# Kernel tuning notes

Measured on AMD Instinct MI355X. Metric: run time of the kernel, lower is better.

## Reference

```python
import jax, jax.numpy as jnp
import numpy as np


def setup_inputs() -> dict:
    key = jax.random.key(0)
    ks = jax.random.split(key, 10)
    B, C1, C2, Co, H, W = 4, 128, 128, 128, 64, 64
    Cin = C1 + C2
    delta_p_processed = jax.random.normal(ks[0], (B, C1, H, W), jnp.float32)
    delta_f_hist = jax.random.normal(ks[1], (B, C2, H, W), jnp.float32)
    Wq = jax.random.normal(ks[2], (Co, Cin), jnp.float32) * 0.02
    bq = jax.random.normal(ks[3], (Co,), jnp.float32) * 0.02
    Wk = jax.random.normal(ks[4], (Co, Cin), jnp.float32) * 0.02
    bk = jax.random.normal(ks[5], (Co,), jnp.float32) * 0.02
    Wv = jax.random.normal(ks[6], (Co, Cin), jnp.float32) * 0.02
    bv = jax.random.normal(ks[7], (Co,), jnp.float32) * 0.02
    Wg = jax.random.normal(ks[8], (Co, Co), jnp.float32) * 0.02
    bg = jnp.zeros((Co,), jnp.float32)
    gamma = jnp.array([0.5], jnp.float32)
    return {
        "delta_p_processed": delta_p_processed,
        "delta_f_hist": delta_f_hist,
        "Wq": Wq, "bq": bq, "Wk": Wk, "bk": bk,
        "Wv": Wv, "bv": bv, "Wg": Wg, "bg": bg,
        "gamma": gamma,
    }


def reference(delta_p_processed, delta_f_hist, Wq, bq, Wk, bk, Wv, bv, Wg, bg, gamma):
    x = jnp.concatenate([delta_p_processed, delta_f_hist], axis=1)  # (B, Cin, H, W)
    B, Cin, H, W = x.shape
    Co = Wq.shape[0]
    N = H * W
    xf = x.reshape(B, Cin, N)
    # 1x1 convs == per-pixel linear projections
    q = jnp.einsum('oc,bcn->bno', Wq, xf) + bq          # (B, N, Co)
    k = jnp.einsum('oc,bcn->bon', Wk, xf) + bk[:, None]  # (B, Co, N)
    v = jnp.einsum('oc,bcn->bno', Wv, xf) + bv          # (B, N, Co)
    scale = 1.0 / (Co ** 0.5)
    attn = jax.nn.softmax(jnp.einsum('bno,bom->bnm', q, k) * scale, axis=-1)  # (B, N, N)
    out_attn = jnp.einsum('bnm,bmo->bno', attn, v)      # (B, N, Co)
    out_attn = out_attn.transpose(0, 2, 1).reshape(B, Co, H, W)
    gate = jax.nn.sigmoid(
        jnp.einsum('oc,bchw->bohw', Wg, out_attn) + bg[None, :, None, None]
    )
    residual = x[:, :Co, :, :]
    return gamma[0] * gate * out_attn + (1.0 - gate) * residual
```

## Files before the change

### kernel.cpp

```cpp
#include <hip/hip_runtime.h>
#include <stdint.h>

#define B_    4
#define CIN   256
#define CO    128
#define NPOS  4096

typedef float  f4      __attribute__((ext_vector_type(4)));
typedef float  f2      __attribute__((ext_vector_type(2)));
typedef float  f32x16  __attribute__((ext_vector_type(16)));
typedef int    int4v   __attribute__((ext_vector_type(4)));
typedef short  short4v __attribute__((ext_vector_type(4)));
typedef short  short8v __attribute__((ext_vector_type(8)));
typedef __bf16 bf16x8  __attribute__((ext_vector_type(8)));

#if __has_builtin(__builtin_amdgcn_exp2f)
#define EXP2(x) __builtin_amdgcn_exp2f(x)
#else
#define EXP2(x) exp2f(x)
#endif

static __device__ __forceinline__ unsigned short f2bf(float f){
  union { float f; unsigned int u; } v; v.f = f;
  unsigned int u = v.u + 0x7FFFu + ((v.u >> 16) & 1u);
  return (unsigned short)(u >> 16);
}
static __device__ __forceinline__ float bf2f(unsigned short h){
  union { unsigned int u; float f; } v; v.u = ((unsigned int)h) << 16;
  return v.f;
}
static __device__ __forceinline__ unsigned int cvt_pk_bf16(float lo, float hi){
  unsigned int r;
  asm("v_cvt_pk_bf16_f32 %0, %1, %2" : "=v"(r) : "v"(lo), "v"(hi));
  return r;
}

static __device__ __forceinline__ void half_swap_pair(float v, float& x, float& y){
  union { float f; int i; } a; a.f = v;
  auto r = __builtin_amdgcn_permlane32_swap(a.i, a.i, false, false);
  union { int i; float f; } o0, o1; o0.i = (int)r[0]; o1.i = (int)r[1];
  x = o0.f; y = o1.f;
}

__global__ __launch_bounds__(64) void wconv_kernel(
    const float* __restrict__ Wq, const float* __restrict__ Wk,
    const float* __restrict__ Wv, const float* __restrict__ Wg,
    unsigned short* __restrict__ Wf)
{
  int blk = blockIdx.x, l = threadIdx.x;
  const float* W; int o, c; int stride;
  if (blk < 192){
    int ob = blk >> 4, cs = blk & 15;
    int mat = ob >> 2, obl = ob & 3;
    W = (mat == 0) ? Wq : ((mat == 1) ? Wk : Wv);
    o = obl * 32 + (l & 31); c = cs * 16 + (l >> 5) * 8; stride = 256;
  } else {
    int idx = blk - 192;
    int ob = idx >> 3, cs = idx & 7;
    W = Wg;
    o = ob * 32 + (l & 31); c = cs * 16 + (l >> 5) * 8; stride = 128;
  }
  const float* src = W + (size_t)o * stride + c;
  f4 a = *(const f4*)src, bb = *(const f4*)(src + 4);
  short8v pk;
  #pragma unroll
  for (int j = 0; j < 4; ++j){ pk[j] = (short)f2bf(a[j]); pk[4+j] = (short)f2bf(bb[j]); }
  *(short8v*)(Wf + ((size_t)blk * 64 + l) * 8) = pk;
}

__global__ __launch_bounds__(256) void qkv_kernel(
    const float* __restrict__ dp, const float* __restrict__ df,
    const unsigned short* __restrict__ Wf,
    const float* __restrict__ bq, const float* __restrict__ bk,
    const float* __restrict__ bv,
    unsigned short* __restrict__ Qf, unsigned short* __restrict__ Kf,
    unsigned short* __restrict__ Vf)
{
  __shared__ unsigned int xs4[32 * 128];

  int t  = threadIdx.x;
  int b  = blockIdx.x >> 7;
  int kt = blockIdx.x & 127;
  int n0 = kt * 32;

  {
    int cp = t & 127, nh = t >> 7;
    int c0 = cp * 2, c1 = c0 + 1;
    const float* s0 = (c0 < 128) ? dp + ((size_t)b*128 + c0) * NPOS
                                 : df + ((size_t)b*128 + (c0-128)) * NPOS;
    const float* s1 = (c1 < 128) ? dp + ((size_t)b*128 + c1) * NPOS
                                 : df + ((size_t)b*128 + (c1-128)) * NPOS;
    f4 x0[4], x1[4];
    #pragma unroll
    for (int i = 0; i < 4; ++i){
      x0[i] = *(const f4*)(s0 + n0 + nh*16 + i*4);
      x1[i] = *(const f4*)(s1 + n0 + nh*16 + i*4);
    }
    #pragma unroll
    for (int i = 0; i < 16; ++i){
      int n = nh * 16 + i;
      unsigned int pk = cvt_pk_bf16(x0[i>>2][i&3], x1[i>>2][i&3]);
      int chunk = (cp >> 2) ^ (n & 7);
      xs4[n * 128 + chunk * 4 + (cp & 3)] = pk;
    }
  }
  __syncthreads();

  int w = t >> 6, l = t & 63;
  int lo5 = l & 31, h = l >> 5;

  f32x16 acc[3] = {};
  const unsigned short* WfL = Wf + (size_t)l * 8;

  #pragma unroll 4
  for (int cs = 0; cs < 16; ++cs){
    bf16x8 xf = *(const bf16x8*)((const char*)xs4 +
                 (size_t)(lo5 * 512 + (((cs*2 + h) ^ (lo5 & 7)) * 16)));
    #pragma unroll
    for (int i = 0; i < 3; ++i){
      int ob = w * 3 + i;
      bf16x8 wf = *(const bf16x8*)(WfL + ((size_t)ob * 16 + cs) * 512);
      if (ob < 8) acc[i] = __builtin_amdgcn_mfma_f32_32x32x16_bf16(wf, xf, acc[i], 0, 0, 0);
      else        acc[i] = __builtin_amdgcn_mfma_f32_32x32x16_bf16(xf, wf, acc[i], 0, 0, 0);
    }
  }

  const float kScale = 0.12751743f;
  #pragma unroll
  for (int i = 0; i < 3; ++i){
    int ob = w * 3 + i, mat = ob >> 2, obl = ob & 3;
    if (mat < 2){
      const float* bias = (mat == 0) ? bq : bk;
      unsigned short* dst = ((mat == 0) ? Qf : Kf) + (size_t)(b*128 + kt) * 4096;
      #pragma unroll
      for (int r1 = 0; r1 < 4; ++r1){
        f4 b4 = *(const f4*)(bias + obl*32 + r1*8 + h*4);
        float v0 = acc[i][r1*4+0] + b4[0], v1 = acc[i][r1*4+1] + b4[1];
        float v2 = acc[i][r1*4+2] + b4[2], v3 = acc[i][r1*4+3] + b4[3];
        if (mat == 0){ v0 *= kScale; v1 *= kScale; v2 *= kScale; v3 *= kScale; }
        union { unsigned int u[2]; short4v s; } pk;
        pk.u[0] = cvt_pk_bf16(v0, v1); pk.u[1] = cvt_pk_bf16(v2, v3);
        int ci = obl * 2 + (r1 >> 1);
        size_t si = (size_t)ci * 512 + (size_t)(lo5 + 32*(r1 & 1)) * 8 + 4*h;
        *(short4v*)(dst + si) = pk.s;
      }
    } else {
      float bvl = bv[obl * 32 + lo5];
      unsigned short* dst = Vf + ((size_t)(b*128 + kt) * 8 + obl*2) * 512;
      #pragma unroll
      for (int r1 = 0; r1 < 4; ++r1){
        union { unsigned int u[2]; short4v s; } pk;
        pk.u[0] = cvt_pk_bf16(acc[i][r1*4+0] + bvl, acc[i][r1*4+1] + bvl);
        pk.u[1] = cvt_pk_bf16(acc[i][r1*4+2] + bvl, acc[i][r1*4+3] + bvl);
        size_t si = (size_t)(r1 >> 1) * 512 + (size_t)(lo5 + 32*(r1 & 1)) * 8 + 4*h;
        *(short4v*)(dst + si) = pk.s;
      }
    }
  }
}

#define PIPE_TILE(T, CUR, NXT)                                                  \
  {                                                                             \
                 \
    {                                                                           \
      int t2_ = (T) + 2; if (t2_ >= NIT) t2_ -= NIT;                            \
      int t1_ = (T) + 1; if (t1_ >= NIT) t1_ -= NIT;                            \
      size_t tbK_ = (size_t)(kt0 + t2_) * 4096;                                 \
      size_t tbV_ = (size_t)(kt0 + t1_) * 4096;                                 \
      _Pragma("unroll")                                                         \
      for (int ci = 0; ci < 8; ++ci)                                            \
        kf[NXT][ci] = *(const bf16x8*)(KfL + tbK_ + ci * 512);                  \
      _Pragma("unroll")                                                         \
      for (int fi = 0; fi < 8; ++fi)                                            \
        vf[NXT][fi] = *(const bf16x8*)(VfL + tbV_ + fi * 512);                  \
    }                                                                           \
                    \
    f32x16 sA = {}, sB = {};                                                    \
    __builtin_amdgcn_s_setprio(1);                                              \
    _Pragma("unroll")                                                           \
    for (int ci = 0; ci < 4; ++ci){                                             \
      sA = __builtin_amdgcn_mfma_f32_32x32x16_bf16(kf[CUR][2*ci],   qf[2*ci],   sA, 0, 0, 0); \
      sB = __builtin_amdgcn_mfma_f32_32x32x16_bf16(kf[CUR][2*ci+1], qf[2*ci+1], sB, 0, 0, 0); \
    }                                                                           \
    __builtin_amdgcn_s_setprio(0);                                              \
         \
    float a0_ = fmaxf(fmaxf(sv[0],  sv[1]),  sv[2]);                            \
    float a1_ = fmaxf(fmaxf(sv[3],  sv[4]),  sv[5]);                            \
    float a2_ = fmaxf(fmaxf(sv[6],  sv[7]),  sv[8]);                            \
    float a3_ = fmaxf(fmaxf(sv[9],  sv[10]), sv[11]);                           \
    float a4_ = fmaxf(fmaxf(sv[12], sv[13]), sv[14]);                           \
    float vm  = fmaxf(fmaxf(fmaxf(fmaxf(a0_, a1_), a2_), fmaxf(a3_, a4_)), sv[15]); \
    { float xx_, yy_; half_swap_pair(vm, xx_, yy_);                             \
      vm = fmaxf(vm, fmaxf(xx_, yy_)); }                                        \
    if (!__all(vm <= m_run + 8.0f)){                                            \
      float m_new = fmaxf(m_run, vm);                                           \
      float alpha = EXP2(m_run - m_new);                                        \
      _Pragma("unroll")                                                         \
      for (int ob = 0; ob < 4; ++ob){                                           \
        _Pragma("unroll")                                                       \
        for (int i = 0; i < 16; ++i) oacc[ob][i] *= alpha;                      \
      }                                                                         \
      l_run *= alpha;                                                           \
      m_run = m_new;                                                            \
    }                                                                           \
    float p[16];                                                                \
    _Pragma("unroll")                                                           \
    for (int i = 0; i < 16; ++i) p[i] = EXP2(sv[i] - m_run);                    \
    float t0 = (p[0]  + p[1])  + (p[2]  + p[3]);                                \
    float t1 = (p[4]  + p[5])  + (p[6]  + p[7]);                                \
    float t2 = (p[8]  + p[9])  + (p[10] + p[11]);                               \
    float t3 = (p[12] + p[13]) + (p[14] + p[15]);                               \
    float ts = (t0 + t1) + (t2 + t3);                                           \
    { float xx_, yy_; half_swap_pair(ts, xx_, yy_); ts = xx_ + yy_; }           \
    l_run += ts;                                                                \
    unsigned int pw[8];                                                         \
    _Pragma("unroll")                                                           \
    for (int i = 0; i < 8; ++i) pw[i] = cvt_pk_bf16(p[2*i], p[2*i+1]);          \
    auto r20 = __builtin_amdgcn_permlane32_swap((int)pw[2], (int)pw[0], false, false); \
    auto r31 = __builtin_amdgcn_permlane32_swap((int)pw[3], (int)pw[1], false, false); \
    auto r64v = __builtin_amdgcn_permlane32_swap((int)pw[6], (int)pw[4], false, false); \
    auto r75 = __builtin_amdgcn_permlane32_swap((int)pw[7], (int)pw[5], false, false); \
    union { int4v i4; bf16x8 b; } pb0, pb1;                                     \
    pb0.i4 = (int4v){(int)r20[1],  (int)r31[1], (int)r20[0],  (int)r31[0]};     \
    pb1.i4 = (int4v){(int)r64v[1], (int)r75[1], (int)r64v[0], (int)r75[0]};     \
                                                     \
    __builtin_amdgcn_s_setprio(1);                                              \
    _Pragma("unroll")                                                           \
    for (int ob = 0; ob < 4; ++ob){                                             \
      oacc[ob] = __builtin_amdgcn_mfma_f32_32x32x16_bf16(vf[CUR][2*ob],   pb0.b, oacc[ob], 0, 0, 0); \
      oacc[ob] = __builtin_amdgcn_mfma_f32_32x32x16_bf16(vf[CUR][2*ob+1], pb1.b, oacc[ob], 0, 0, 0); \
    }                                                                           \
    __builtin_amdgcn_s_setprio(0);                                              \
              \
    sv = sA + sB;                                                               \
  }

__global__ __launch_bounds__(256) void attn_kernel(
    const unsigned short* __restrict__ Qf, const unsigned short* __restrict__ Kf,
    const unsigned short* __restrict__ Vf, float* __restrict__ OP,
    f2* __restrict__ ML, int SPLIT, int CHUNK)
{
  int t    = threadIdx.x;
  int s    = blockIdx.x % SPLIT;
  int rest = blockIdx.x / SPLIT;
  int b    = rest >> 5;
  int qb   = rest & 31;
  int w    = t >> 6;
  int l    = t & 63;
  int lq   = l & 31;
  int h    = l >> 5;
  int q0   = qb * 128 + w * 32;

  const unsigned short* QfL = Qf + (size_t)b * (128 * 8 * 512) + (size_t)l * 8;
  size_t qtb = (size_t)(q0 >> 5) * 4096;
  bf16x8 qf[8];
  #pragma unroll
  for (int ci = 0; ci < 8; ++ci) qf[ci] = *(const bf16x8*)(QfL + qtb + ci * 512);

  const unsigned short* KfL = Kf + (size_t)b * (128 * 8 * 512) + (size_t)l * 8;
  const unsigned short* VfL = Vf + (size_t)b * (128 * 8 * 512) + (size_t)l * 8;

  f32x16 oacc[4] = {};
  float m_run = -3.0e38f, l_run = 0.f;

  const int kt0 = (s * CHUNK) >> 5;
  const int NIT = CHUNK >> 5;

  bf16x8 kf[2][8];
  bf16x8 vf[2][8];
  {
    size_t tb0 = (size_t)kt0 * 4096;
    #pragma unroll
    for (int ci = 0; ci < 8; ++ci) kf[1][ci] = *(const bf16x8*)(KfL + tb0 + ci * 512);
    #pragma unroll
    for (int fi = 0; fi < 8; ++fi) vf[0][fi] = *(const bf16x8*)(VfL + tb0 + fi * 512);
    size_t tb1 = (size_t)(kt0 + 1) * 4096;
    #pragma unroll
    for (int ci = 0; ci < 8; ++ci) kf[0][ci] = *(const bf16x8*)(KfL + tb1 + ci * 512);
  }
  f32x16 sv;
  {
    f32x16 sA = {}, sB = {};
    #pragma unroll
    for (int ci = 0; ci < 4; ++ci){
      sA = __builtin_amdgcn_mfma_f32_32x32x16_bf16(kf[1][2*ci],   qf[2*ci],   sA, 0, 0, 0);
      sB = __builtin_amdgcn_mfma_f32_32x32x16_bf16(kf[1][2*ci+1], qf[2*ci+1], sB, 0, 0, 0);
    }
    sv = sA + sB;
  }

  for (int it = 0; it < NIT; it += 2){
    PIPE_TILE(it, 0, 1)
    PIPE_TILE(it + 1, 1, 0)
  }

  float* Ob = OP + (((size_t)b * NPOS + q0 + lq) * SPLIT + s) * 128 + h * 4;
  #pragma unroll
  for (int ob = 0; ob < 4; ++ob){
    #pragma unroll
    for (int rg = 0; rg < 4; ++rg){
      f4 vv;
      vv[0] = oacc[ob][rg*4+0]; vv[1] = oacc[ob][rg*4+1];
      vv[2] = oacc[ob][rg*4+2]; vv[3] = oacc[ob][rg*4+3];
      *(f4*)(Ob + ob * 32 + rg * 8) = vv;
    }
  }
  if (h == 0){
    f2 ml; ml[0] = m_run; ml[1] = l_run;
    ML[((size_t)b * NPOS + q0 + lq) * SPLIT + s] = ml;
  }
}

__global__ __launch_bounds__(256) void gate_kernel(
    const float* __restrict__ OP, const f2* __restrict__ ML,
    const unsigned short* __restrict__ Wf,
    const float* __restrict__ bg,
    const float* __restrict__ gamma, const float* __restrict__ dp,
    float* __restrict__ out, int SPLIT)
{
  __shared__ float        oat[128 * 33];
  __shared__ unsigned int xs[32 * 64];
  __shared__ float        wsm[32 * 8];

  int t  = threadIdx.x;
  int b  = blockIdx.x >> 7;
  int nt = blockIdx.x & 127;
  int n0 = nt * 32;

  if (t < 32){
    size_t mlb = ((size_t)b * NPOS + n0 + t) * SPLIT;
    float mmax = -3.0e38f;
    for (int sp = 0; sp < SPLIT; ++sp) mmax = fmaxf(mmax, ML[mlb + sp][0]);
    float L = 0.f;
    for (int sp = 0; sp < SPLIT; ++sp) L += ML[mlb + sp][1] * EXP2(ML[mlb + sp][0] - mmax);
    float Linv = 1.0f / L;
    for (int sp = 0; sp < SPLIT; ++sp)
      wsm[t * 8 + sp] = EXP2(ML[mlb + sp][0] - mmax) * Linv;
  }
  __syncthreads();

  int w = t >> 6, l = t & 63;

  #pragma unroll
  for (int i = 0; i < 8; ++i){
    int n = w * 8 + i;
    const f2* op = (const f2*)(OP + (((size_t)b * NPOS + n0 + n) * SPLIT) * 128) + l;
    float a0 = 0.f, a1 = 0.f;
    for (int sp = 0; sp < SPLIT; ++sp){
      f2 v = op[sp * 64];
      float ww = wsm[n * 8 + sp];
      a0 += ww * v[0]; a1 += ww * v[1];
    }
    oat[(2*l)   * 33 + n] = a0;
    oat[(2*l+1) * 33 + n] = a1;
    xs[n * 64 + (((l >> 2) ^ (n & 7)) << 2) + (l & 3)] = cvt_pk_bf16(a0, a1);
  }
  __syncthreads();

  int lq = l & 31, h = l >> 5;
  f32x16 acc = {};
  const unsigned short* WgfL = Wf + (size_t)(192 + w * 8) * 512 + (size_t)l * 8;
  #pragma unroll
  for (int cs = 0; cs < 8; ++cs){
    bf16x8 xf = *(const bf16x8*)((const char*)xs +
                 (size_t)(lq * 256 + (((cs*2 + h) ^ (lq & 7)) * 16)));
    bf16x8 wgf = *(const bf16x8*)(WgfL + (size_t)cs * 512);
    acc = __builtin_amdgcn_mfma_f32_32x32x16_bf16(wgf, xf, acc, 0, 0, 0);
  }

  float gm = gamma[0];
  const float kLog2e = 1.4426950408889634f;
  #pragma unroll
  for (int r1 = 0; r1 < 4; ++r1){
    f4 b4 = *(const f4*)(bg + w*32 + r1*8 + h*4);
    #pragma unroll
    for (int j = 0; j < 4; ++j){
      int o = w*32 + r1*8 + h*4 + j;
      float garg = acc[r1*4 + j] + b4[j];
      float gate = 1.0f / (1.0f + EXP2(-kLog2e * garg));
      float oa = oat[o * 33 + lq];
      size_t gi = ((size_t)b * 128 + o) * NPOS + n0 + lq;
      float rs = dp[gi];
      out[gi] = gm * gate * oa + (1.0f - gate) * rs;
    }
  }
}

extern "C" void kernel_launch(void* const* d_in, const int* in_sizes, int n_in,
                              void* d_out, int out_size, void* d_ws, size_t ws_size,
                              hipStream_t stream)
{
  (void)in_sizes; (void)n_in; (void)out_size;
  const float* dp    = (const float*)d_in[0];
  const float* df    = (const float*)d_in[1];
  const float* Wq    = (const float*)d_in[2];
  const float* bq    = (const float*)d_in[3];
  const float* Wk    = (const float*)d_in[4];
  const float* bk    = (const float*)d_in[5];
  const float* Wv    = (const float*)d_in[6];
  const float* bv    = (const float*)d_in[7];
  const float* Wg    = (const float*)d_in[8];
  const float* bg    = (const float*)d_in[9];
  const float* gamma = (const float*)d_in[10];

  const int SPLIT = 4;
  const int CHUNK = NPOS / SPLIT;

  unsigned short* Qf = (unsigned short*)d_ws;
  unsigned short* Kf = Qf + (size_t)B_ * NPOS * 128;
  unsigned short* Vf = Kf + (size_t)B_ * NPOS * 128;
  float*          OP = (float*)(Vf + (size_t)B_ * NPOS * 128);
  f2*             ML = (f2*)(OP + (size_t)B_ * NPOS * SPLIT * 128);
  unsigned short* Wf = (unsigned short*)(ML + (size_t)B_ * NPOS * SPLIT);
  float*          out = (float*)d_out;
  (void)ws_size;

  wconv_kernel<<<dim3(224), dim3(64), 0, stream>>>(Wq, Wk, Wv, Wg, Wf);
  qkv_kernel<<<dim3(B_ * 128), dim3(256), 0, stream>>>(dp, df, Wf, bq, bk, bv, Qf, Kf, Vf);
  attn_kernel<<<dim3(B_ * 32 * SPLIT), dim3(256), 0, stream>>>(Qf, Kf, Vf, OP, ML, SPLIT, CHUNK);
  gate_kernel<<<dim3(B_ * 128), dim3(256), 0, stream>>>(OP, ML, Wf, bg, gamma, dp, out, SPLIT);
}
```

Baseline: 94.56 us.

## Process two key tiles per iteration and compute softmax row sums via MFMA

Replaces the software-pipelined single-tile loop, which prefetched the next K and V tiles into register double buffers, with an unpipelined loop that handles two key tiles per iteration and shares one max/rescale check between them. The softmax denominator is now accumulated by extra MFMAs against a ones vector on the bf16 probabilities, replacing the scalar sums and cross-lane reductions. This cuts VALU reduction work and per-tile control overhead, but it loses the explicit load/compute overlap and adds MFMA work and register pressure. The row sum now uses bf16-rounded probabilities, which slightly changes numerics.

After: 99.93 us. 5.7% more time.

```diff
diff --git a/kernel.cpp b/kernel.cpp
--- a/kernel.cpp
+++ b/kernel.cpp
@@ -159,82 +159,6 @@
   }
 }
 
-#define PIPE_TILE(T, CUR, NXT)                                                  \
-  {                                                                             \
-                 \
-    {                                                                           \
-      int t2_ = (T) + 2; if (t2_ >= NIT) t2_ -= NIT;                            \
-      int t1_ = (T) + 1; if (t1_ >= NIT) t1_ -= NIT;                            \
-      size_t tbK_ = (size_t)(kt0 + t2_) * 4096;                                 \
-      size_t tbV_ = (size_t)(kt0 + t1_) * 4096;                                 \
-      _Pragma("unroll")                                                         \
-      for (int ci = 0; ci < 8; ++ci)                                            \
-        kf[NXT][ci] = *(const bf16x8*)(KfL + tbK_ + ci * 512);                  \
-      _Pragma("unroll")                                                         \
-      for (int fi = 0; fi < 8; ++fi)                                            \
-        vf[NXT][fi] = *(const bf16x8*)(VfL + tbV_ + fi * 512);                  \
-    }                                                                           \
-                    \
-    f32x16 sA = {}, sB = {};                                                    \
-    __builtin_amdgcn_s_setprio(1);                                              \
-    _Pragma("unroll")                                                           \
-    for (int ci = 0; ci < 4; ++ci){                                             \
-      sA = __builtin_amdgcn_mfma_f32_32x32x16_bf16(kf[CUR][2*ci],   qf[2*ci],   sA, 0, 0, 0); \
-      sB = __builtin_amdgcn_mfma_f32_32x32x16_bf16(kf[CUR][2*ci+1], qf[2*ci+1], sB, 0, 0, 0); \
-    }                                                                           \
-    __builtin_amdgcn_s_setprio(0);                                              \
-         \
-    float a0_ = fmaxf(fmaxf(sv[0],  sv[1]),  sv[2]);                            \
-    float a1_ = fmaxf(fmaxf(sv[3],  sv[4]),  sv[5]);                            \
-    float a2_ = fmaxf(fmaxf(sv[6],  sv[7]),  sv[8]);                            \
-    float a3_ = fmaxf(fmaxf(sv[9],  sv[10]), sv[11]);                           \
-    float a4_ = fmaxf(fmaxf(sv[12], sv[13]), sv[14]);                           \
-    float vm  = fmaxf(fmaxf(fmaxf(fmaxf(a0_, a1_), a2_), fmaxf(a3_, a4_)), sv[15]); \
-    { float xx_, yy_; half_swap_pair(vm, xx_, yy_);                             \
-      vm = fmaxf(vm, fmaxf(xx_, yy_)); }                                        \
-    if (!__all(vm <= m_run + 8.0f)){                                            \
-      float m_new = fmaxf(m_run, vm);                                           \
-      float alpha = EXP2(m_run - m_new);                                        \
-      _Pragma("unroll")                                                         \
-      for (int ob = 0; ob < 4; ++ob){                                           \
-        _Pragma("unroll")                                                       \
-        for (int i = 0; i < 16; ++i) oacc[ob][i] *= alpha;                      \
-      }                                                                         \
-      l_run *= alpha;                                                           \
-      m_run = m_new;                                                            \
-    }                                                                           \
-    float p[16];                                                                \
-    _Pragma("unroll")                                                           \
-    for (int i = 0; i < 16; ++i) p[i] = EXP2(sv[i] - m_run);                    \
-    float t0 = (p[0]  + p[1])  + (p[2]  + p[3]);                                \
-    float t1 = (p[4]  + p[5])  + (p[6]  + p[7]);                                \
-    float t2 = (p[8]  + p[9])  + (p[10] + p[11]);                               \
-    float t3 = (p[12] + p[13]) + (p[14] + p[15]);                               \
-    float ts = (t0 + t1) + (t2 + t3);                                           \
-    { float xx_, yy_; half_swap_pair(ts, xx_, yy_); ts = xx_ + yy_; }           \
-    l_run += ts;                                                                \
-    unsigned int pw[8];                                                         \
-    _Pragma("unroll")                                                           \
-    for (int i = 0; i < 8; ++i) pw[i] = cvt_pk_bf16(p[2*i], p[2*i+1]);          \
-    auto r20 = __builtin_amdgcn_permlane32_swap((int)pw[2], (int)pw[0], false, false); \
-    auto r31 = __builtin_amdgcn_permlane32_swap((int)pw[3], (int)pw[1], false, false); \
-    auto r64v = __builtin_amdgcn_permlane32_swap((int)pw[6], (int)pw[4], false, false); \
-    auto r75 = __builtin_amdgcn_permlane32_swap((int)pw[7], (int)pw[5], false, false); \
-    union { int4v i4; bf16x8 b; } pb0, pb1;                                     \
-    pb0.i4 = (int4v){(int)r20[1],  (int)r31[1], (int)r20[0],  (int)r31[0]};     \
-    pb1.i4 = (int4v){(int)r64v[1], (int)r75[1], (int)r64v[0], (int)r75[0]};     \
-                                                     \
-    __builtin_amdgcn_s_setprio(1);                                              \
-    _Pragma("unroll")                                                           \
-    for (int ob = 0; ob < 4; ++ob){                                             \
-      oacc[ob] = __builtin_amdgcn_mfma_f32_32x32x16_bf16(vf[CUR][2*ob],   pb0.b, oacc[ob], 0, 0, 0); \
-      oacc[ob] = __builtin_amdgcn_mfma_f32_32x32x16_bf16(vf[CUR][2*ob+1], pb1.b, oacc[ob], 0, 0, 0); \
-    }                                                                           \
-    __builtin_amdgcn_s_setprio(0);                                              \
-              \
-    sv = sA + sB;                                                               \
-  }
-
 __global__ __launch_bounds__(256) void attn_kernel(
     const unsigned short* __restrict__ Qf, const unsigned short* __restrict__ Kf,
     const unsigned short* __restrict__ Vf, float* __restrict__ OP,
@@ -261,37 +185,119 @@
   const unsigned short* VfL = Vf + (size_t)b * (128 * 8 * 512) + (size_t)l * 8;
 
   f32x16 oacc[4] = {};
-  float m_run = -3.0e38f, l_run = 0.f;
+  f32x16 lacc = {};
+  float m_run = -3.0e38f;
+
+  union { int4v i4; bf16x8 b; } ones_u;
+  ones_u.i4 = (int4v){0x3F803F80, 0x3F803F80, 0x3F803F80, 0x3F803F80};
+  bf16x8 ones = ones_u.b;
 
   const int kt0 = (s * CHUNK) >> 5;
   const int NIT = CHUNK >> 5;
 
-  bf16x8 kf[2][8];
-  bf16x8 vf[2][8];
-  {
-    size_t tb0 = (size_t)kt0 * 4096;
-    #pragma unroll
-    for (int ci = 0; ci < 8; ++ci) kf[1][ci] = *(const bf16x8*)(KfL + tb0 + ci * 512);
-    #pragma unroll
-    for (int fi = 0; fi < 8; ++fi) vf[0][fi] = *(const bf16x8*)(VfL + tb0 + fi * 512);
-    size_t tb1 = (size_t)(kt0 + 1) * 4096;
-    #pragma unroll
-    for (int ci = 0; ci < 8; ++ci) kf[0][ci] = *(const bf16x8*)(KfL + tb1 + ci * 512);
-  }
-  f32x16 sv;
-  {
-    f32x16 sA = {}, sB = {};
-    #pragma unroll
-    for (int ci = 0; ci < 4; ++ci){
-      sA = __builtin_amdgcn_mfma_f32_32x32x16_bf16(kf[1][2*ci],   qf[2*ci],   sA, 0, 0, 0);
-      sB = __builtin_amdgcn_mfma_f32_32x32x16_bf16(kf[1][2*ci+1], qf[2*ci+1], sB, 0, 0, 0);
-    }
-    sv = sA + sB;
-  }
-
   for (int it = 0; it < NIT; it += 2){
-    PIPE_TILE(it, 0, 1)
-    PIPE_TILE(it + 1, 1, 0)
+    size_t tbA = (size_t)(kt0 + it) * 4096;
+    size_t tbB = tbA + 4096;
+
+    bf16x8 kfA[8], kfB[8];
+    #pragma unroll
+    for (int ci = 0; ci < 8; ++ci){
+      kfA[ci] = *(const bf16x8*)(KfL + tbA + ci * 512);
+      kfB[ci] = *(const bf16x8*)(KfL + tbB + ci * 512);
+    }
+    f32x16 svA = {}, svB = {};
+    __builtin_amdgcn_s_setprio(1);
+    #pragma unroll
+    for (int ci = 0; ci < 8; ++ci){
+      svA = __builtin_amdgcn_mfma_f32_32x32x16_bf16(kfA[ci], qf[ci], svA, 0, 0, 0);
+      svB = __builtin_amdgcn_mfma_f32_32x32x16_bf16(kfB[ci], qf[ci], svB, 0, 0, 0);
+    }
+    __builtin_amdgcn_s_setprio(0);
+
+    bf16x8 vfA[8], vfB[8];
+    #pragma unroll
+    for (int fi = 0; fi < 8; ++fi){
+      vfA[fi] = *(const bf16x8*)(VfL + tbA + fi * 512);
+      vfB[fi] = *(const bf16x8*)(VfL + tbB + fi * 512);
+    }
+
+    float mA, mB;
+    { float a0_ = fmaxf(fmaxf(svA[0],  svA[1]),  svA[2]);
+      float a1_ = fmaxf(fmaxf(svA[3],  svA[4]),  svA[5]);
+      float a2_ = fmaxf(fmaxf(svA[6],  svA[7]),  svA[8]);
+      float a3_ = fmaxf(fmaxf(svA[9],  svA[10]), svA[11]);
+      float a4_ = fmaxf(fmaxf(svA[12], svA[13]), svA[14]);
+      mA = fmaxf(fmaxf(fmaxf(fmaxf(a0_, a1_), a2_), fmaxf(a3_, a4_)), svA[15]); }
+    { float a0_ = fmaxf(fmaxf(svB[0],  svB[1]),  svB[2]);
+      float a1_ = fmaxf(fmaxf(svB[3],  svB[4]),  svB[5]);
+      float a2_ = fmaxf(fmaxf(svB[6],  svB[7]),  svB[8]);
+      float a3_ = fmaxf(fmaxf(svB[9],  svB[10]), svB[11]);
+      float a4_ = fmaxf(fmaxf(svB[12], svB[13]), svB[14]);
+      mB = fmaxf(fmaxf(fmaxf(fmaxf(a0_, a1_), a2_), fmaxf(a3_, a4_)), svB[15]); }
+    float vm = fmaxf(mA, mB);
+    { float xx_, yy_; half_swap_pair(vm, xx_, yy_);
+      vm = fmaxf(vm, fmaxf(xx_, yy_)); }
+    if (!__all(vm <= m_run + 8.0f)){
+      float m_new = fmaxf(m_run, vm);
+      float alpha = EXP2(m_run - m_new);
+      #pragma unroll
+      for (int ob = 0; ob < 4; ++ob){
+        #pragma unroll
+        for (int i = 0; i < 16; ++i) oacc[ob][i] *= alpha;
+      }
+      #pragma unroll
+      for (int i = 0; i < 16; ++i) lacc[i] *= alpha;
+      m_run = m_new;
+    }
+
+    float pA[16], pB[16];
+    #pragma unroll
+    for (int i = 0; i < 16; ++i){
+      pA[i] = EXP2(svA[i] - m_run);
+      pB[i] = EXP2(svB[i] - m_run);
+    }
+
+    bf16x8 pbA0, pbA1, pbB0, pbB1;
+    {
+      unsigned int pw[8];
+      #pragma unroll
+      for (int i = 0; i < 8; ++i) pw[i] = cvt_pk_bf16(pA[2*i], pA[2*i+1]);
+      auto r20 = __builtin_amdgcn_permlane32_swap((int)pw[2], (int)pw[0], false, false);
+      auto r31 = __builtin_amdgcn_permlane32_swap((int)pw[3], (int)pw[1], false, false);
+      auto r64v = __builtin_amdgcn_permlane32_swap((int)pw[6], (int)pw[4], false, false);
+      auto r75 = __builtin_amdgcn_permlane32_swap((int)pw[7], (int)pw[5], false, false);
+      union { int4v i4; bf16x8 b; } u0, u1;
+      u0.i4 = (int4v){(int)r20[1],  (int)r31[1], (int)r20[0],  (int)r31[0]};
+      u1.i4 = (int4v){(int)r64v[1], (int)r75[1], (int)r64v[0], (int)r75[0]};
+      pbA0 = u0.b; pbA1 = u1.b;
+    }
+    {
+      unsigned int pw[8];
+      #pragma unroll
+      for (int i = 0; i < 8; ++i) pw[i] = cvt_pk_bf16(pB[2*i], pB[2*i+1]);
+      auto r20 = __builtin_amdgcn_permlane32_swap((int)pw[2], (int)pw[0], false, false);
+      auto r31 = __builtin_amdgcn_permlane32_swap((int)pw[3], (int)pw[1], false, false);
+      auto r64v = __builtin_amdgcn_permlane32_swap((int)pw[6], (int)pw[4], false, false);
+      auto r75 = __builtin_amdgcn_permlane32_swap((int)pw[7], (int)pw[5], false, false);
+      union { int4v i4; bf16x8 b; } u0, u1;
+      u0.i4 = (int4v){(int)r20[1],  (int)r31[1], (int)r20[0],  (int)r31[0]};
+      u1.i4 = (int4v){(int)r64v[1], (int)r75[1], (int)r64v[0], (int)r75[0]};
+      pbB0 = u0.b; pbB1 = u1.b;
+    }
+
+    __builtin_amdgcn_s_setprio(1);
+    #pragma unroll
+    for (int ob = 0; ob < 4; ++ob){
+      oacc[ob] = __builtin_amdgcn_mfma_f32_32x32x16_bf16(vfA[2*ob],   pbA0, oacc[ob], 0, 0, 0);
+      oacc[ob] = __builtin_amdgcn_mfma_f32_32x32x16_bf16(vfA[2*ob+1], pbA1, oacc[ob], 0, 0, 0);
+      oacc[ob] = __builtin_amdgcn_mfma_f32_32x32x16_bf16(vfB[2*ob],   pbB0, oacc[ob], 0, 0, 0);
+      oacc[ob] = __builtin_amdgcn_mfma_f32_32x32x16_bf16(vfB[2*ob+1], pbB1, oacc[ob], 0, 0, 0);
+    }
+    lacc = __builtin_amdgcn_mfma_f32_32x32x16_bf16(ones, pbA0, lacc, 0, 0, 0);
+    lacc = __builtin_amdgcn_mfma_f32_32x32x16_bf16(ones, pbA1, lacc, 0, 0, 0);
+    lacc = __builtin_amdgcn_mfma_f32_32x32x16_bf16(ones, pbB0, lacc, 0, 0, 0);
+    lacc = __builtin_amdgcn_mfma_f32_32x32x16_bf16(ones, pbB1, lacc, 0, 0, 0);
+    __builtin_amdgcn_s_setprio(0);
   }
 
   float* Ob = OP + (((size_t)b * NPOS + q0 + lq) * SPLIT + s) * 128 + h * 4;
@@ -306,7 +312,7 @@
     }
   }
   if (h == 0){
-    f2 ml; ml[0] = m_run; ml[1] = l_run;
+    f2 ml; ml[0] = m_run; ml[1] = lacc[0];
     ML[((size_t)b * NPOS + q0 + lq) * SPLIT + s] = ml;
   }
 }
```
